# Performance work log

Measured on AMD Instinct MI355X. Metric: run time of the kernel, lower is better.

Reference implementation:

```python
import jax, jax.numpy as jnp
import numpy as np

EPS = 1e-5
HEADS, DQK, DV, SD = 1, 12, 12, 2  # heads, dim_qk, dim_v, spatial_down


def group_norm(x, w, b):
    # GroupNorm(1, C): normalize over all non-batch dims, per-channel affine
    axes = tuple(range(1, x.ndim))
    m = x.mean(axis=axes, keepdims=True)
    v = x.var(axis=axes, keepdims=True)
    xn = (x - m) * jax.lax.rsqrt(v + EPS)
    shp = (1, -1) + (1,) * (x.ndim - 2)
    return xn * w.reshape(shp) + b.reshape(shp)


def setup_inputs() -> dict:
    key = jax.random.key(0)
    ks = jax.random.split(key, 6)
    B, Ccv, D, H, W = 4, 32, 48, 64, 128
    Cf, Hs, Ws = 256, 8, 16  # Hs*Ws = 128 == max_tokens -> token_pool is identity
    cost = jax.random.normal(ks[0], (B, Ccv, D, H, W), jnp.float32)
    feat_s4 = jax.random.normal(ks[1], (B, Cf, Hs, Ws), jnp.float32)
    E = HEADS * DQK
    w_q = jax.random.normal(ks[2], (E, Ccv), jnp.float32) * (1.0 / np.sqrt(Ccv))
    w_k = jax.random.normal(ks[3], (E, Cf), jnp.float32) * (1.0 / np.sqrt(Cf))
    w_v = jax.random.normal(ks[4], (HEADS * DV, Cf), jnp.float32) * (1.0 / np.sqrt(Cf))
    w_out = jax.random.normal(ks[5], (Ccv, HEADS * DV), jnp.float32) * (1.0 / np.sqrt(HEADS * DV))
    return {
        'cost': cost, 'feat_s4': feat_s4,
        'w_q': w_q, 'w_k': w_k, 'w_v': w_v, 'w_out': w_out,
        'gn_in_w': jnp.ones((Ccv,), jnp.float32), 'gn_in_b': jnp.zeros((Ccv,), jnp.float32),
        'gn_out_w': jnp.ones((Ccv,), jnp.float32), 'gn_out_b': jnp.zeros((Ccv,), jnp.float32),
        'gamma': jnp.float32(0.1),
    }


def reference(cost, feat_s4, w_q, w_k, w_v, w_out, gn_in_w, gn_in_b, gn_out_w, gn_out_b, gamma):
    B, Ccv, D, H, W = cost.shape
    x_in = group_norm(cost, gn_in_w, gn_in_b)
    # avg_pool3d kernel/stride (1, SD, SD)
    Hq, Wq = H // SD, W // SD
    xq = x_in.reshape(B, Ccv, D, Hq, SD, Wq, SD).mean(axis=(4, 6))
    # 1x1 conv projections == channel matmuls
    q = jnp.einsum('bcdhw,ec->bedhw', xq, w_q)          # (B, h*dqk, D, Hq, Wq)
    k = jnp.einsum('bchw,ec->behw', feat_s4, w_k)       # (B, h*dqk, Hs, Ws)
    v = jnp.einsum('bchw,ec->behw', feat_s4, w_v)       # (B, h*dv, Hs, Ws)
    Ns = k.shape[2] * k.shape[3]
    kf = k.reshape(B, HEADS, DQK, Ns)                   # (B, h, dqk, Ns)
    vf = v.reshape(B, HEADS, DV, Ns)                    # (B, h, dv, Ns)
    N = D * Hq * Wq
    qf = q.reshape(B, HEADS, DQK, N).transpose(0, 1, 3, 2)  # (B, h, N, dqk)
    logits = jnp.einsum('bhnq,bhqs->bhns', qf, kf) * (DQK ** -0.5)
    attn = jax.nn.softmax(logits, axis=-1)
    out = jnp.einsum('bhns,bhds->bhnd', attn, vf)       # (B, h, N, dv)
    out = out.transpose(0, 1, 3, 2).reshape(B, HEADS * DV, D, Hq, Wq)
    out = jnp.einsum('bedhw,ce->bcdhw', out, w_out)     # (B, Ccv, D, Hq, Wq)
    # trilinear upsample (align_corners=False == half-pixel, jax.image default)
    out = jax.image.resize(out, (B, Ccv, D, H, W), method='trilinear')
    out = out.astype(jnp.bfloat16).astype(jnp.float32)  # replicate torch bf16 cast
    return group_norm(cost + gamma * out, gn_out_w, gn_out_b)
```

## Files before the change

### kernel.cpp

```cpp
#include <hip/hip_runtime.h>

typedef float f4v __attribute__((ext_vector_type(4)));

namespace {
constexpr int Bn = 4, Cn = 32, Dn = 48, Hn = 64, Wn = 128;
constexpr int HQ = 32, WQ = 64;
constexpr int NPB = Dn * HQ * WQ;
constexpr int DHW = Dn * Hn * Wn;
constexpr int PERB = Cn * DHW;
constexpr int NS = 128, En = 12;
constexpr float EPS = 1e-5f;
constexpr float SQK = 0.2886751345948129f;

constexpr size_t OFF_Z    = 0;
constexpr size_t OFF_QR   = 6291456;
constexpr size_t OFF_P1   = OFF_QR + 2359296;
constexpr size_t OFF_P2   = OFF_P1 + 16384;
constexpr size_t OFF_ST1  = OFF_P2 + 12288;
constexpr size_t OFF_ST2  = OFF_ST1 + 8;
constexpr size_t OFF_KB   = OFF_ST2 + 8;
constexpr size_t OFF_VB   = OFF_KB + 6144;
constexpr size_t OFF_KS   = OFF_VB + 6144;
constexpr size_t OFF_PKV  = OFF_KS + 4;
}

__device__ inline unsigned short bf16b(float x) {
    unsigned u = __float_as_uint(x);
    return (unsigned short)((u + 0x7fffu + ((u >> 16) & 1u)) >> 16);
}
__device__ inline float b2f(unsigned short h) { return __uint_as_float(((unsigned)h) << 16); }
__device__ inline float bf16_rne(float x) {
    unsigned u = __float_as_uint(x);
    u = (u + 0x7fffu + ((u >> 16) & 1u)) & 0xffff0000u;
    return __uint_as_float(u);
}

__device__ inline float2 block_red2(float s, float ss) {
#pragma unroll
    for (int off = 32; off; off >>= 1) {
        s += __shfl_down(s, off, 64);
        ss += __shfl_down(ss, off, 64);
    }
    __shared__ float red[8];
    int lane = threadIdx.x & 63, w = threadIdx.x >> 6;
    if (!lane) { red[w] = s; red[4 + w] = ss; }
    __syncthreads();
    float2 r = make_float2(red[0] + red[1] + red[2] + red[3],
                           red[4] + red[5] + red[6] + red[7]);
    __syncthreads();
    return r;
}

__global__ __launch_bounds__(256) void k1_pool(const float* __restrict__ cost,
                                               const float* __restrict__ feat,
                                               const float* __restrict__ w_q,
                                               const float* __restrict__ w_k,
                                               const float* __restrict__ w_v,
                                               const float* __restrict__ gniw,
                                               unsigned short* __restrict__ qr,
                                               float2* __restrict__ part1,
                                               float* __restrict__ pkv) {
    __shared__ float wqg[En * Cn];
    const int b = blockIdx.y, tid = threadIdx.x;
    for (int i = tid; i < En * Cn; i += 256) wqg[i] = w_q[i] * gniw[i & 31];
    __syncthreads();
    const int n = blockIdx.x * 256 + tid;
    const int d = n >> 11, r = n & 2047, hq = r >> 6, wq = r & 63;
    const float* base = cost + (size_t)b * PERB + (size_t)d * 8192 + (hq * 2) * Wn + wq * 2;
    float s = 0.f, ss = 0.f;
    float q[En];
#pragma unroll
    for (int e = 0; e < En; ++e) q[e] = 0.f;
#pragma unroll 4
    for (int c = 0; c < Cn; ++c) {
        const float* src = base + (size_t)c * DHW;
        float2 t0 = *reinterpret_cast<const float2*>(src);
        float2 t1 = *reinterpret_cast<const float2*>(src + Wn);
        float ps = t0.x + t0.y + t1.x + t1.y;
        s += ps;
        ss += t0.x * t0.x + t0.y * t0.y + t1.x * t1.x + t1.y * t1.y;
        float pv = 0.25f * ps;
#pragma unroll
        for (int e = 0; e < En; ++e) q[e] += wqg[e * Cn + c] * pv;
    }
#pragma unroll
    for (int e = 0; e < En; ++e) qr[(size_t)(b * En + e) * NPB + n] = bf16b(q[e]);
    float2 rp = block_red2(s, ss);
    if (!tid) part1[b * 2048 + blockIdx.x] = rp;

    if (b == 0 && blockIdx.x < 64 && tid < NS) {
        const int kb = blockIdx.x >> 4, ch = blockIdx.x & 15, sI = tid;
        float f[16];
#pragma unroll
        for (int j = 0; j < 16; ++j) f[j] = feat[(size_t)(kb * 256 + ch * 16 + j) * NS + sI];
        float kk[En], vv[En];
#pragma unroll
        for (int e = 0; e < En; ++e) { kk[e] = 0.f; vv[e] = 0.f; }
#pragma unroll
        for (int j = 0; j < 16; ++j) {
            const int c = ch * 16 + j;
#pragma unroll
            for (int e = 0; e < En; ++e) {
                kk[e] += w_k[e * 256 + c] * f[j];
                vv[e] += w_v[e * 256 + c] * f[j];
            }
        }
#pragma unroll
        for (int e = 0; e < En; ++e) {
            pkv[((size_t)(kb * 16 + ch) * 24 + e) * 128 + sI] = kk[e];
            pkv[((size_t)(kb * 16 + ch) * 24 + 12 + e) * 128 + sI] = vv[e];
        }
    }
}

__global__ __launch_bounds__(256) void k_mid(const float2* __restrict__ part1,
                                             const float* __restrict__ pkv,
                                             float2* __restrict__ st1,
                                             float* __restrict__ KB, float* __restrict__ VB,
                                             float* __restrict__ ksc) {
    const int blk = blockIdx.x, tid = threadIdx.x;
    if (blk < 4) {
        float s = 0.f, ss = 0.f;
        for (int i = tid; i < 384; i += 256) {
            float2 v = part1[blk * 2048 + i];
            s += v.x; ss += v.y;
        }
        float2 t = block_red2(s, ss);
        if (!tid) {
            float m = t.x / (float)PERB;
            float var = t.y / (float)PERB - m * m;
            st1[blk] = make_float2(m, rsqrtf(var + EPS));
        }
    } else {
        const int b = blk - 4;
        __shared__ float wmax[2];
        if (tid < NS) {
            const int s = tid;
            float kk[En], vv[En];
#pragma unroll
            for (int e = 0; e < En; ++e) { kk[e] = 0.f; vv[e] = 0.f; }
            for (int ch = 0; ch < 16; ++ch) {
                const float* p = pkv + ((size_t)(b * 16 + ch) * 24) * 128 + s;
#pragma unroll
                for (int e = 0; e < En; ++e) {
                    kk[e] += p[e * 128];
                    vv[e] += p[(12 + e) * 128];
                }
            }
            float n2 = 0.f;
#pragma unroll
            for (int e = 0; e < En; ++e) {
                KB[(size_t)(b * NS + s) * En + e] = kk[e];
                VB[(size_t)(b * NS + s) * En + e] = vv[e];
                n2 += kk[e] * kk[e];
            }
            float nn = sqrtf(n2);
#pragma unroll
            for (int off = 32; off; off >>= 1) nn = fmaxf(nn, __shfl_down(nn, off, 64));
            if (!(tid & 63)) wmax[tid >> 6] = nn;
        }
        __syncthreads();
        if (!tid) ksc[b] = fmaxf(wmax[0], wmax[1]);
    }
}

__global__ __launch_bounds__(256) void k_attn(const unsigned short* __restrict__ qr,
                                              const float* __restrict__ KB,
                                              const float* __restrict__ VB,
                                              const float* __restrict__ w_q,
                                              const float* __restrict__ gniw,
                                              const float* __restrict__ gnib,
                                              const float* __restrict__ ksc,
                                              const float2* __restrict__ st1,
                                              const float* __restrict__ w_out,
                                              unsigned short* __restrict__ zb) {
    __shared__ float Ks[NS * En], Vs[NS * En], WOs[Cn * En], QBs[En];
    const int b = blockIdx.y, tid = threadIdx.x;
    for (int i = tid; i < NS * En; i += 256) {
        Ks[i] = KB[(size_t)b * NS * En + i];
        Vs[i] = VB[(size_t)b * NS * En + i];
    }
    for (int i = tid; i < Cn * En; i += 256) WOs[i] = w_out[i];
    float2 s1 = st1[b];
    if (tid < En) {
        float acc = 0.f;
        for (int c = 0; c < Cn; ++c)
            acc += w_q[tid * Cn + c] * (gnib[c] - s1.x * s1.y * gniw[c]);
        QBs[tid] = SQK * acc;
    }
    __syncthreads();
    const int n = blockIdx.x * 256 + tid;
    const float qsc = s1.y * SQK;
    float q[En];
    float qn2 = 0.f;
#pragma unroll
    for (int e = 0; e < En; ++e) {
        q[e] = qsc * b2f(qr[(size_t)(b * En + e) * NPB + n]) + QBs[e];
        qn2 += q[e] * q[e];
    }
    const float ub = sqrtf(qn2) * ksc[b];
    float l = 0.f;
    float o[En];
#pragma unroll
    for (int e = 0; e < En; ++e) o[e] = 0.f;
    for (int s = 0; s < NS; ++s) {
        float dot = 0.f;
#pragma unroll
        for (int e = 0; e < En; ++e) dot += q[e] * Ks[s * En + e];
        float pe = __expf(dot - ub);
        l += pe;
#pragma unroll
        for (int e = 0; e < En; ++e) o[e] += pe * Vs[s * En + e];
    }
    const float inv = 1.0f / l;
    for (int c = 0; c < Cn; ++c) {
        float z = 0.f;
#pragma unroll
        for (int e = 0; e < En; ++e) z += WOs[c * En + e] * o[e];
        zb[(size_t)(b * Cn + c) * NPB + n] = bf16b(z * inv);
    }
}

__global__ __launch_bounds__(256) void k_ystats(const float* __restrict__ cost,
                                                const unsigned short* __restrict__ zb,
                                                const float* __restrict__ gamma_p,
                                                float2* __restrict__ part2) {
    const int blk = blockIdx.x;
    __shared__ unsigned short zs[HQ * WQ];
    const int tid = threadIdx.x;
    {
        const unsigned int* zsrc = (const unsigned int*)(zb + (size_t)blk * 2048);
        for (int i = tid; i < 1024; i += 256) ((unsigned int*)zs)[i] = zsrc[i];
    }
    __syncthreads();
    const float g = gamma_p[0];
    const f4v* cq = (const f4v*)(cost + (size_t)blk * 8192);
    float s = 0.f, ss = 0.f;
#pragma unroll
    for (int k = 0; k < 8; ++k) {
        int qd = tid + 256 * k;
        int h = qd >> 5, w4 = (qd & 31) << 2;
        f4v cv = cq[qd];
        int h0 = (h - 1) >> 1;
        float wh0 = (h & 1) ? 0.75f : 0.25f;
        int h1 = h0 + 1;
        h0 = h0 < 0 ? 0 : h0; h1 = h1 > HQ - 1 ? HQ - 1 : h1;
        const unsigned short* r0 = zs + h0 * WQ;
        const unsigned short* r1 = zs + h1 * WQ;
#pragma unroll
        for (int j = 0; j < 4; ++j) {
            int w = w4 + j;
            int w0 = (w - 1) >> 1;
            float ww0 = (w & 1) ? 0.75f : 0.25f;
            int w1 = w0 + 1;
            w0 = w0 < 0 ? 0 : w0; w1 = w1 > WQ - 1 ? WQ - 1 : w1;
            float u = wh0 * (ww0 * b2f(r0[w0]) + (1.f - ww0) * b2f(r0[w1])) +
                      (1.f - wh0) * (ww0 * b2f(r1[w0]) + (1.f - ww0) * b2f(r1[w1]));
            float y = cv[j] + g * bf16_rne(u);
            s += y; ss += y * y;
        }
    }
    float2 rp = block_red2(s, ss);
    if (!tid) part2[blk] = rp;
}

__global__ __launch_bounds__(256) void k_fin2(const float2* __restrict__ part2,
                                              float2* __restrict__ st2) {
    const int b = blockIdx.x, tid = threadIdx.x;
    float s = 0.f, ss = 0.f;
    for (int i = tid; i < 1536; i += 256) {
        float2 v = part2[b * 1536 + i];
        s += v.x; ss += v.y;
    }
    float2 t = block_red2(s, ss);
    if (!tid) {
        float m = t.x / (float)PERB;
        float var = t.y / (float)PERB - m * m;
        st2[b] = make_float2(m, rsqrtf(var + EPS));
    }
}

__global__ __launch_bounds__(256) void k_final(const float* __restrict__ cost,
                                               const unsigned short* __restrict__ zb,
                                               const float* __restrict__ gamma_p,
                                               const float2* __restrict__ st2,
                                               const float* __restrict__ gow,
                                               const float* __restrict__ gob,
                                               float* __restrict__ out) {
    const int blk = blockIdx.x;
    __shared__ unsigned short zs[HQ * WQ];
    const int tid = threadIdx.x;
    {
        const unsigned int* zsrc = (const unsigned int*)(zb + (size_t)blk * 2048);
        for (int i = tid; i < 1024; i += 256) ((unsigned int*)zs)[i] = zsrc[i];
    }
    __syncthreads();
    const int b = blk / (Cn * Dn);
    const int c = (blk / Dn) % Cn;
    const float g = gamma_p[0];
    float2 st = st2[b];
    const float m = st.x, sc = st.y * gow[c], bi = gob[c];
    const f4v* cq = (const f4v*)(cost + (size_t)blk * 8192);
    f4v* oq = (f4v*)(out + (size_t)blk * 8192);
#pragma unroll
    for (int k = 0; k < 8; ++k) {
        int qd = tid + 256 * k;
        int h = qd >> 5, w4 = (qd & 31) << 2;
        f4v cv = cq[qd];
        int h0 = (h - 1) >> 1;
        float wh0 = (h & 1) ? 0.75f : 0.25f;
        int h1 = h0 + 1;
        h0 = h0 < 0 ? 0 : h0; h1 = h1 > HQ - 1 ? HQ - 1 : h1;
        const unsigned short* r0 = zs + h0 * WQ;
        const unsigned short* r1 = zs + h1 * WQ;
        f4v ov;
#pragma unroll
        for (int j = 0; j < 4; ++j) {
            int w = w4 + j;
            int w0 = (w - 1) >> 1;
            float ww0 = (w & 1) ? 0.75f : 0.25f;
            int w1 = w0 + 1;
            w0 = w0 < 0 ? 0 : w0; w1 = w1 > WQ - 1 ? WQ - 1 : w1;
            float u = wh0 * (ww0 * b2f(r0[w0]) + (1.f - ww0) * b2f(r0[w1])) +
                      (1.f - wh0) * (ww0 * b2f(r1[w0]) + (1.f - ww0) * b2f(r1[w1]));
            float y = cv[j] + g * bf16_rne(u);
            ov[j] = (y - m) * sc + bi;
        }
        __builtin_nontemporal_store(ov, oq + qd);
    }
}

extern "C" void kernel_launch(void* const* d_in, const int* in_sizes, int n_in,
                              void* d_out, int out_size, void* d_ws, size_t ws_size,
                              hipStream_t stream) {
    const float* cost  = (const float*)d_in[0];
    const float* feat  = (const float*)d_in[1];
    const float* w_q   = (const float*)d_in[2];
    const float* w_k   = (const float*)d_in[3];
    const float* w_v   = (const float*)d_in[4];
    const float* w_out = (const float*)d_in[5];
    const float* gniw  = (const float*)d_in[6];
    const float* gnib  = (const float*)d_in[7];
    const float* gow   = (const float*)d_in[8];
    const float* gob   = (const float*)d_in[9];
    const float* gamma = (const float*)d_in[10];

    float* ws = (float*)d_ws;
    float* outp = (float*)d_out;

    unsigned short* zb = (unsigned short*)(ws + OFF_Z);
    unsigned short* qr = (unsigned short*)(ws + OFF_QR);
    float2* part1 = (float2*)(ws + OFF_P1);
    float2* part2 = (float2*)(ws + OFF_P2);
    float2* st1 = (float2*)(ws + OFF_ST1);
    float2* st2 = (float2*)(ws + OFF_ST2);
    float* KB  = ws + OFF_KB;
    float* VB  = ws + OFF_VB;
    float* ksc = ws + OFF_KS;
    float* pkv = ws + OFF_PKV;

    k1_pool<<<dim3(384, Bn), 256, 0, stream>>>(cost, feat, w_q, w_k, w_v, gniw, qr, part1, pkv);
    k_mid<<<8, 256, 0, stream>>>(part1, pkv, st1, KB, VB, ksc);
    k_attn<<<dim3(384, Bn), 256, 0, stream>>>(qr, KB, VB, w_q, gniw, gnib, ksc, st1, w_out, zb);
    k_ystats<<<Bn * Cn * Dn, 256, 0, stream>>>(cost, zb, gamma, part2);
    k_fin2<<<Bn, 256, 0, stream>>>(part2, st2);
    k_final<<<Bn * Cn * Dn, 256, 0, stream>>>(cost, zb, gamma, st2, gow, gob, outp);
}
```

Baseline: 198.5 us.

## Fuse attention with output-stats pass and fold reductions into last-block atomics

Splits the K/V projection into its own small kernel, and folds the GroupNorm statistics finalization into the last block of the pooling kernel using an atomic counter. The attention kernel now also computes the upsampled y statistics from a shared-memory tile, recomputing halo rows of attention locally, which removes the separate ystats and fin2 kernels and k_mid. This saves several launches and one full pass that reread zb, at the cost of redundant halo attention work, more shared memory per block, and serialized last-block reductions.

```diff
diff --git a/kernel.cpp b/kernel.cpp
--- a/kernel.cpp
+++ b/kernel.cpp
@@ -11,17 +11,16 @@
 constexpr int NS = 128, En = 12;
 constexpr float EPS = 1e-5f;
 constexpr float SQK = 0.2886751345948129f;
-
-constexpr size_t OFF_Z    = 0;
-constexpr size_t OFF_QR   = 6291456;
-constexpr size_t OFF_P1   = OFF_QR + 2359296;
-constexpr size_t OFF_P2   = OFF_P1 + 16384;
-constexpr size_t OFF_ST1  = OFF_P2 + 12288;
-constexpr size_t OFF_ST2  = OFF_ST1 + 8;
-constexpr size_t OFF_KB   = OFF_ST2 + 8;
-constexpr size_t OFF_VB   = OFF_KB + 6144;
-constexpr size_t OFF_KS   = OFF_VB + 6144;
-constexpr size_t OFF_PKV  = OFF_KS + 4;
+constexpr int NBLK = 384;
+
+constexpr size_t OFF_ZB  = 0;
+constexpr size_t OFF_QR  = 6291456;
+constexpr size_t OFF_P1  = OFF_QR + 2359296;
+constexpr size_t OFF_P2  = OFF_P1 + 3072;
+constexpr size_t OFF_ST1 = OFF_P2 + 3072;
+constexpr size_t OFF_ST2 = OFF_ST1 + 8;
+constexpr size_t OFF_PKV = OFF_ST2 + 8;
+constexpr size_t OFF_CNT = OFF_PKV + 49152;
 }
 
 __device__ inline unsigned short bf16b(float x) {
@@ -43,24 +42,56 @@
     }
     __shared__ float red[8];
     int lane = threadIdx.x & 63, w = threadIdx.x >> 6;
+    __syncthreads();
     if (!lane) { red[w] = s; red[4 + w] = ss; }
     __syncthreads();
-    float2 r = make_float2(red[0] + red[1] + red[2] + red[3],
-                           red[4] + red[5] + red[6] + red[7]);
-    __syncthreads();
-    return r;
+    return make_float2(red[0] + red[1] + red[2] + red[3],
+                       red[4] + red[5] + red[6] + red[7]);
+}
+
+__global__ __launch_bounds__(128) void k_kv(const float* __restrict__ feat,
+                                            const float* __restrict__ w_k,
+                                            const float* __restrict__ w_v,
+                                            float* __restrict__ pkv,
+                                            unsigned* __restrict__ cnt) {
+    const int g = blockIdx.x;
+    const int s = threadIdx.x;
+    if (g == 0 && s < 2) cnt[s] = 0;
+    const int kb = g >> 2, cg = g & 3;
+    float kk[En], vv[En];
+#pragma unroll
+    for (int e = 0; e < En; ++e) { kk[e] = 0.f; vv[e] = 0.f; }
+    for (int ch = 0; ch < 4; ++ch) {
+        const int c0 = cg * 64 + ch * 16;
+        float f[16];
+#pragma unroll
+        for (int jj = 0; jj < 16; ++jj) f[jj] = feat[(size_t)(kb * 256 + c0 + jj) * NS + s];
+#pragma unroll
+        for (int jj = 0; jj < 16; ++jj) {
+            const int c = c0 + jj;
+#pragma unroll
+            for (int e = 0; e < En; ++e) {
+                kk[e] += w_k[e * 256 + c] * f[jj];
+                vv[e] += w_v[e * 256 + c] * f[jj];
+            }
+        }
+    }
+#pragma unroll
+    for (int e = 0; e < En; ++e) {
+        pkv[((size_t)(g * NS + s)) * 24 + e] = kk[e];
+        pkv[((size_t)(g * NS + s)) * 24 + 12 + e] = vv[e];
+    }
 }
 
 __global__ __launch_bounds__(256) void k1_pool(const float* __restrict__ cost,
-                                               const float* __restrict__ feat,
                                                const float* __restrict__ w_q,
-                                               const float* __restrict__ w_k,
-                                               const float* __restrict__ w_v,
                                                const float* __restrict__ gniw,
                                                unsigned short* __restrict__ qr,
                                                float2* __restrict__ part1,
-                                               float* __restrict__ pkv) {
+                                               float2* __restrict__ st1,
+                                               unsigned* __restrict__ cnt) {
     __shared__ float wqg[En * Cn];
+    __shared__ unsigned lastf;
     const int b = blockIdx.y, tid = threadIdx.x;
     for (int i = tid; i < En * Cn; i += 256) wqg[i] = w_q[i] * gniw[i & 31];
     __syncthreads();
@@ -86,102 +117,55 @@
 #pragma unroll
     for (int e = 0; e < En; ++e) qr[(size_t)(b * En + e) * NPB + n] = bf16b(q[e]);
     float2 rp = block_red2(s, ss);
-    if (!tid) part1[b * 2048 + blockIdx.x] = rp;
-
-    if (b == 0 && blockIdx.x < 64 && tid < NS) {
-        const int kb = blockIdx.x >> 4, ch = blockIdx.x & 15, sI = tid;
-        float f[16];
-#pragma unroll
-        for (int j = 0; j < 16; ++j) f[j] = feat[(size_t)(kb * 256 + ch * 16 + j) * NS + sI];
-        float kk[En], vv[En];
-#pragma unroll
-        for (int e = 0; e < En; ++e) { kk[e] = 0.f; vv[e] = 0.f; }
-#pragma unroll
-        for (int j = 0; j < 16; ++j) {
-            const int c = ch * 16 + j;
-#pragma unroll
-            for (int e = 0; e < En; ++e) {
-                kk[e] += w_k[e * 256 + c] * f[j];
-                vv[e] += w_v[e * 256 + c] * f[j];
-            }
-        }
-#pragma unroll
-        for (int e = 0; e < En; ++e) {
-            pkv[((size_t)(kb * 16 + ch) * 24 + e) * 128 + sI] = kk[e];
-            pkv[((size_t)(kb * 16 + ch) * 24 + 12 + e) * 128 + sI] = vv[e];
-        }
-    }
-}
-
-__global__ __launch_bounds__(256) void k_mid(const float2* __restrict__ part1,
-                                             const float* __restrict__ pkv,
-                                             float2* __restrict__ st1,
-                                             float* __restrict__ KB, float* __restrict__ VB,
-                                             float* __restrict__ ksc) {
-    const int blk = blockIdx.x, tid = threadIdx.x;
-    if (blk < 4) {
-        float s = 0.f, ss = 0.f;
-        for (int i = tid; i < 384; i += 256) {
-            float2 v = part1[blk * 2048 + i];
-            s += v.x; ss += v.y;
-        }
-        float2 t = block_red2(s, ss);
-        if (!tid) {
-            float m = t.x / (float)PERB;
-            float var = t.y / (float)PERB - m * m;
-            st1[blk] = make_float2(m, rsqrtf(var + EPS));
-        }
-    } else {
-        const int b = blk - 4;
-        __shared__ float wmax[2];
-        if (tid < NS) {
-            const int s = tid;
-            float kk[En], vv[En];
-#pragma unroll
-            for (int e = 0; e < En; ++e) { kk[e] = 0.f; vv[e] = 0.f; }
-            for (int ch = 0; ch < 16; ++ch) {
-                const float* p = pkv + ((size_t)(b * 16 + ch) * 24) * 128 + s;
-#pragma unroll
-                for (int e = 0; e < En; ++e) {
-                    kk[e] += p[e * 128];
-                    vv[e] += p[(12 + e) * 128];
-                }
-            }
-            float n2 = 0.f;
-#pragma unroll
-            for (int e = 0; e < En; ++e) {
-                KB[(size_t)(b * NS + s) * En + e] = kk[e];
-                VB[(size_t)(b * NS + s) * En + e] = vv[e];
-                n2 += kk[e] * kk[e];
-            }
-            float nn = sqrtf(n2);
-#pragma unroll
-            for (int off = 32; off; off >>= 1) nn = fmaxf(nn, __shfl_down(nn, off, 64));
-            if (!(tid & 63)) wmax[tid >> 6] = nn;
-        }
-        __syncthreads();
-        if (!tid) ksc[b] = fmaxf(wmax[0], wmax[1]);
-    }
-}
-
-__global__ __launch_bounds__(256) void k_attn(const unsigned short* __restrict__ qr,
-                                              const float* __restrict__ KB,
-                                              const float* __restrict__ VB,
-                                              const float* __restrict__ w_q,
-                                              const float* __restrict__ gniw,
-                                              const float* __restrict__ gnib,
-                                              const float* __restrict__ ksc,
-                                              const float2* __restrict__ st1,
-                                              const float* __restrict__ w_out,
-                                              unsigned short* __restrict__ zb) {
+    if (!tid) part1[b * NBLK + blockIdx.x] = rp;
+
+    __threadfence();
+    if (!tid) { unsigned old = atomicAdd(cnt, 1u); lastf = (old == 4u * NBLK - 1u); }
+    __syncthreads();
+    if (lastf) {
+        __threadfence();
+        for (int bb = 0; bb < 4; ++bb) {
+            float s2 = 0.f, ss2 = 0.f;
+            for (int i = tid; i < NBLK; i += 256) {
+                float2 v = part1[bb * NBLK + i];
+                s2 += v.x; ss2 += v.y;
+            }
+            float2 t = block_red2(s2, ss2);
+            if (!tid) {
+                float m = t.x / (float)PERB;
+                float var = t.y / (float)PERB - m * m;
+                st1[bb] = make_float2(m, rsqrtf(var + EPS));
+            }
+        }
+    }
+}
+
+__global__ __launch_bounds__(256) void k_attn_ystats(
+    const float* __restrict__ cost, const unsigned short* __restrict__ qr,
+    const float* __restrict__ pkv, const float* __restrict__ w_q,
+    const float* __restrict__ gniw, const float* __restrict__ gnib,
+    const float2* __restrict__ st1, const float* __restrict__ w_out,
+    const float* __restrict__ gamma_p,
+    unsigned short* __restrict__ zb, float2* __restrict__ part2,
+    float2* __restrict__ st2, unsigned* __restrict__ cnt) {
     __shared__ float Ks[NS * En], Vs[NS * En], WOs[Cn * En], QBs[En];
-    const int b = blockIdx.y, tid = threadIdx.x;
+    __shared__ float plB[128 * 13];
+    __shared__ unsigned short zsl[Cn * 6 * 64];
+    __shared__ float kred[2];
+    __shared__ float kscs_sh;
+    __shared__ unsigned lastf;
+
+    const int x = blockIdx.x, b = blockIdx.y, tid = threadIdx.x;
+    const int d = x >> 3, j = x & 7;
+
     for (int i = tid; i < NS * En; i += 256) {
-        Ks[i] = KB[(size_t)b * NS * En + i];
-        Vs[i] = VB[(size_t)b * NS * En + i];
+        int s = i / En, e = i - s * En;
+        size_t base = ((size_t)((b * 4) * NS + s)) * 24 + e;
+        Ks[i] = pkv[base] + pkv[base + 3072] + pkv[base + 6144] + pkv[base + 9216];
+        Vs[i] = pkv[base + 12] + pkv[base + 3084] + pkv[base + 6156] + pkv[base + 9228];
     }
     for (int i = tid; i < Cn * En; i += 256) WOs[i] = w_out[i];
-    float2 s1 = st1[b];
+    const float2 s1 = st1[b];
     if (tid < En) {
         float acc = 0.f;
         for (int c = 0; c < Cn; ++c)
@@ -189,94 +173,155 @@
         QBs[tid] = SQK * acc;
     }
     __syncthreads();
-    const int n = blockIdx.x * 256 + tid;
+    if (tid < NS) {
+        float n2 = 0.f;
+#pragma unroll
+        for (int e = 0; e < En; ++e) { float k = Ks[tid * En + e]; n2 += k * k; }
+#pragma unroll
+        for (int off = 32; off; off >>= 1) n2 = fmaxf(n2, __shfl_down(n2, off, 64));
+        if (!(tid & 63)) kred[tid >> 6] = n2;
+    }
+    __syncthreads();
+    if (!tid) kscs_sh = sqrtf(fmaxf(kred[0], kred[1]));
+    __syncthreads();
+    const float kscs = kscs_sh;
     const float qsc = s1.y * SQK;
-    float q[En];
-    float qn2 = 0.f;
-#pragma unroll
-    for (int e = 0; e < En; ++e) {
-        q[e] = qsc * b2f(qr[(size_t)(b * En + e) * NPB + n]) + QBs[e];
-        qn2 += q[e] * q[e];
-    }
-    const float ub = sqrtf(qn2) * ksc[b];
-    float l = 0.f;
-    float o[En];
-#pragma unroll
-    for (int e = 0; e < En; ++e) o[e] = 0.f;
-    for (int s = 0; s < NS; ++s) {
-        float dot = 0.f;
-#pragma unroll
-        for (int e = 0; e < En; ++e) dot += q[e] * Ks[s * En + e];
-        float pe = __expf(dot - ub);
-        l += pe;
-#pragma unroll
-        for (int e = 0; e < En; ++e) o[e] += pe * Vs[s * En + e];
-    }
-    const float inv = 1.0f / l;
-    for (int c = 0; c < Cn; ++c) {
-        float z = 0.f;
-#pragma unroll
-        for (int e = 0; e < En; ++e) z += WOs[c * En + e] * o[e];
-        zb[(size_t)(b * Cn + c) * NPB + n] = bf16b(z * inv);
-    }
-}
-
-__global__ __launch_bounds__(256) void k_ystats(const float* __restrict__ cost,
-                                                const unsigned short* __restrict__ zb,
-                                                const float* __restrict__ gamma_p,
-                                                float2* __restrict__ part2) {
-    const int blk = blockIdx.x;
-    __shared__ unsigned short zs[HQ * WQ];
-    const int tid = threadIdx.x;
+
     {
-        const unsigned int* zsrc = (const unsigned int*)(zb + (size_t)blk * 2048);
-        for (int i = tid; i < 1024; i += 256) ((unsigned int*)zs)[i] = zsrc[i];
-    }
-    __syncthreads();
-    const float g = gamma_p[0];
-    const f4v* cq = (const f4v*)(cost + (size_t)blk * 8192);
-    float s = 0.f, ss = 0.f;
-#pragma unroll
-    for (int k = 0; k < 8; ++k) {
-        int qd = tid + 256 * k;
-        int h = qd >> 5, w4 = (qd & 31) << 2;
-        f4v cv = cq[qd];
-        int h0 = (h - 1) >> 1;
-        float wh0 = (h & 1) ? 0.75f : 0.25f;
+        const int n = x * 256 + tid;
+        float q[En], qn2 = 0.f;
+#pragma unroll
+        for (int e = 0; e < En; ++e) {
+            q[e] = qsc * b2f(qr[(size_t)(b * En + e) * NPB + n]) + QBs[e];
+            qn2 += q[e] * q[e];
+        }
+        const float ub = sqrtf(qn2) * kscs;
+        float l = 0.f, o[En];
+#pragma unroll
+        for (int e = 0; e < En; ++e) o[e] = 0.f;
+        for (int s = 0; s < NS; ++s) {
+            float dot = 0.f;
+#pragma unroll
+            for (int e = 0; e < En; ++e) dot += q[e] * Ks[s * En + e];
+            float pe = __expf(dot - ub);
+            l += pe;
+#pragma unroll
+            for (int e = 0; e < En; ++e) o[e] += pe * Vs[s * En + e];
+        }
+        const float inv = 1.0f / l;
+        const int lrow = tid >> 6, lw = tid & 63;
+        for (int c = 0; c < Cn; ++c) {
+            float z = 0.f;
+#pragma unroll
+            for (int e = 0; e < En; ++e) z += WOs[c * En + e] * o[e];
+            unsigned short zv = bf16b(z * inv);
+            zb[(size_t)(b * Cn + c) * NPB + n] = zv;
+            zsl[c * 384 + lrow * 64 + lw] = zv;
+        }
+    }
+
+    {
+        const int t = tid & 127, half = tid >> 7;
+        const int which = t >> 6;
+        const int lw = t & 63;
+        const int prow = which ? (4 * j + 4) : (4 * j - 1);
+        const bool valid = which ? (j < 7) : (j > 0);
+        float l = 0.f, o[En];
+#pragma unroll
+        for (int e = 0; e < En; ++e) o[e] = 0.f;
+        if (valid) {
+            const int n = d * 2048 + prow * 64 + lw;
+            float q[En], qn2 = 0.f;
+#pragma unroll
+            for (int e = 0; e < En; ++e) {
+                q[e] = qsc * b2f(qr[(size_t)(b * En + e) * NPB + n]) + QBs[e];
+                qn2 += q[e] * q[e];
+            }
+            const float ub = sqrtf(qn2) * kscs;
+            for (int s = half * 64; s < half * 64 + 64; ++s) {
+                float dot = 0.f;
+#pragma unroll
+                for (int e = 0; e < En; ++e) dot += q[e] * Ks[s * En + e];
+                float pe = __expf(dot - ub);
+                l += pe;
+#pragma unroll
+                for (int e = 0; e < En; ++e) o[e] += pe * Vs[s * En + e];
+            }
+        }
+        if (half) {
+            plB[t * 13] = l;
+#pragma unroll
+            for (int e = 0; e < En; ++e) plB[t * 13 + 1 + e] = o[e];
+        }
+        __syncthreads();
+        if (!half && valid) {
+            l += plB[t * 13];
+#pragma unroll
+            for (int e = 0; e < En; ++e) o[e] += plB[t * 13 + 1 + e];
+            const float inv = 1.0f / l;
+            const int zr = which ? 5 : 4;
+            for (int c = 0; c < Cn; ++c) {
+                float z = 0.f;
+#pragma unroll
+                for (int e = 0; e < En; ++e) z += WOs[c * En + e] * o[e];
+                zsl[c * 384 + zr * 64 + lw] = bf16b(z * inv);
+            }
+        }
+    }
+    __syncthreads();
+
+    float ys = 0.f, yss = 0.f;
+    {
+        const float g = gamma_p[0];
+        const int h = tid >> 5, wqd = tid & 31;
+        const int gh = 8 * j + h;
+        int h0 = (gh - 1) >> 1;
+        const float wh0 = (gh & 1) ? 0.75f : 0.25f;
         int h1 = h0 + 1;
         h0 = h0 < 0 ? 0 : h0; h1 = h1 > HQ - 1 ? HQ - 1 : h1;
-        const unsigned short* r0 = zs + h0 * WQ;
-        const unsigned short* r1 = zs + h1 * WQ;
-#pragma unroll
-        for (int j = 0; j < 4; ++j) {
-            int w = w4 + j;
-            int w0 = (w - 1) >> 1;
-            float ww0 = (w & 1) ? 0.75f : 0.25f;
-            int w1 = w0 + 1;
-            w0 = w0 < 0 ? 0 : w0; w1 = w1 > WQ - 1 ? WQ - 1 : w1;
-            float u = wh0 * (ww0 * b2f(r0[w0]) + (1.f - ww0) * b2f(r0[w1])) +
-                      (1.f - wh0) * (ww0 * b2f(r1[w0]) + (1.f - ww0) * b2f(r1[w1]));
-            float y = cv[j] + g * bf16_rne(u);
-            s += y; ss += y * y;
-        }
-    }
-    float2 rp = block_red2(s, ss);
-    if (!tid) part2[blk] = rp;
-}
-
-__global__ __launch_bounds__(256) void k_fin2(const float2* __restrict__ part2,
-                                              float2* __restrict__ st2) {
-    const int b = blockIdx.x, tid = threadIdx.x;
-    float s = 0.f, ss = 0.f;
-    for (int i = tid; i < 1536; i += 256) {
-        float2 v = part2[b * 1536 + i];
-        s += v.x; ss += v.y;
-    }
-    float2 t = block_red2(s, ss);
-    if (!tid) {
-        float m = t.x / (float)PERB;
-        float var = t.y / (float)PERB - m * m;
-        st2[b] = make_float2(m, rsqrtf(var + EPS));
+        int lr0 = h0 - 4 * j, lr1 = h1 - 4 * j;
+        lr0 = (lr0 < 0) ? 4 : lr0;
+        lr1 = (lr1 > 3) ? 5 : lr1;
+        const float* cbase = cost + (size_t)b * PERB + (size_t)d * 8192 + (size_t)gh * Wn + wqd * 4;
+        for (int c = 0; c < Cn; ++c) {
+            f4v cv = *reinterpret_cast<const f4v*>(cbase + (size_t)c * DHW);
+            const unsigned short* z0 = zsl + c * 384 + lr0 * 64;
+            const unsigned short* z1 = zsl + c * 384 + lr1 * 64;
+#pragma unroll
+            for (int p = 0; p < 4; ++p) {
+                int w = wqd * 4 + p;
+                int w0 = (w - 1) >> 1;
+                float ww0 = (w & 1) ? 0.75f : 0.25f;
+                int w1 = w0 + 1;
+                w0 = w0 < 0 ? 0 : w0; w1 = w1 > WQ - 1 ? WQ - 1 : w1;
+                float u = wh0 * (ww0 * b2f(z0[w0]) + (1.f - ww0) * b2f(z0[w1])) +
+                          (1.f - wh0) * (ww0 * b2f(z1[w0]) + (1.f - ww0) * b2f(z1[w1]));
+                float y = cv[p] + g * bf16_rne(u);
+                ys += y; yss += y * y;
+            }
+        }
+    }
+    float2 rp = block_red2(ys, yss);
+    if (!tid) part2[b * NBLK + x] = rp;
+
+    __threadfence();
+    if (!tid) { unsigned old = atomicAdd(cnt + 1, 1u); lastf = (old == 4u * NBLK - 1u); }
+    __syncthreads();
+    if (lastf) {
+        __threadfence();
+        for (int bb = 0; bb < 4; ++bb) {
+            float s2 = 0.f, ss2 = 0.f;
+            for (int i = tid; i < NBLK; i += 256) {
+                float2 v = part2[bb * NBLK + i];
+                s2 += v.x; ss2 += v.y;
+            }
+            float2 t = block_red2(s2, ss2);
+            if (!tid) {
+                float m = t.x / (float)PERB;
+                float var = t.y / (float)PERB - m * m;
+                st2[bb] = make_float2(m, rsqrtf(var + EPS));
+            }
+        }
     }
 }
 
@@ -315,16 +360,16 @@
         const unsigned short* r1 = zs + h1 * WQ;
         f4v ov;
 #pragma unroll
-        for (int j = 0; j < 4; ++j) {
-            int w = w4 + j;
+        for (int p = 0; p < 4; ++p) {
+            int w = w4 + p;
             int w0 = (w - 1) >> 1;
             float ww0 = (w & 1) ? 0.75f : 0.25f;
             int w1 = w0 + 1;
             w0 = w0 < 0 ? 0 : w0; w1 = w1 > WQ - 1 ? WQ - 1 : w1;
             float u = wh0 * (ww0 * b2f(r0[w0]) + (1.f - ww0) * b2f(r0[w1])) +
                       (1.f - wh0) * (ww0 * b2f(r1[w0]) + (1.f - ww0) * b2f(r1[w1]));
-            float y = cv[j] + g * bf16_rne(u);
-            ov[j] = (y - m) * sc + bi;
+            float y = cv[p] + g * bf16_rne(u);
+            ov[p] = (y - m) * sc + bi;
         }
         __builtin_nontemporal_store(ov, oq + qd);
     }
@@ -348,21 +393,18 @@
     float* ws = (float*)d_ws;
     float* outp = (float*)d_out;
 
-    unsigned short* zb = (unsigned short*)(ws + OFF_Z);
+    unsigned short* zb = (unsigned short*)(ws + OFF_ZB);
     unsigned short* qr = (unsigned short*)(ws + OFF_QR);
     float2* part1 = (float2*)(ws + OFF_P1);
     float2* part2 = (float2*)(ws + OFF_P2);
     float2* st1 = (float2*)(ws + OFF_ST1);
     float2* st2 = (float2*)(ws + OFF_ST2);
-    float* KB  = ws + OFF_KB;
-    float* VB  = ws + OFF_VB;
-    float* ksc = ws + OFF_KS;
     float* pkv = ws + OFF_PKV;
-
-    k1_pool<<<dim3(384, Bn), 256, 0, stream>>>(cost, feat, w_q, w_k, w_v, gniw, qr, part1, pkv);
-    k_mid<<<8, 256, 0, stream>>>(part1, pkv, st1, KB, VB, ksc);
-    k_attn<<<dim3(384, Bn), 256, 0, stream>>>(qr, KB, VB, w_q, gniw, gnib, ksc, st1, w_out, zb);
-    k_ystats<<<Bn * Cn * Dn, 256, 0, stream>>>(cost, zb, gamma, part2);
-    k_fin2<<<Bn, 256, 0, stream>>>(part2, st2);
+    unsigned* cnt = (unsigned*)(ws + OFF_CNT);
+
+    k_kv<<<16, 128, 0, stream>>>(feat, w_k, w_v, pkv, cnt);
+    k1_pool<<<dim3(NBLK, Bn), 256, 0, stream>>>(cost, w_q, gniw, qr, part1, st1, cnt);
+    k_attn_ystats<<<dim3(NBLK, Bn), 256, 0, stream>>>(cost, qr, pkv, w_q, gniw, gnib, st1,
+                                                      w_out, gamma, zb, part2, st2, cnt);
     k_final<<<Bn * Cn * Dn, 256, 0, stream>>>(cost, zb, gamma, st2, gow, gob, outp);
 }
```

After: 589.1 us. 197% more time.
